# Optimization experiments

Hardware: AMD Instinct MI355X
Metric: run time of the kernel (lower is better)

Reference implementation:

```python
import jax, jax.numpy as jnp
import numpy as np

N = 100000      # nodes
E = 1600000     # edges (avg degree 16)
F_IN = 128      # node feature dim
F_E = 8         # edge feature dim
H = 4           # attention heads (layer 1)
C = 16          # hidden per head
T = 1           # target size (layer 2, heads=1, concat=False)
NEG_SLOPE = 0.2


def setup_inputs() -> dict:
    key = jax.random.key(0)
    ks = jax.random.split(key, 20)
    g = lambda k, shape, fan: (jax.random.normal(k, shape, jnp.float32) / np.sqrt(fan))
    return {
        "x": jax.random.normal(ks[0], (N, F_IN), jnp.float32),
        "edge_index": jax.random.randint(ks[1], (2, E), 0, N, dtype=jnp.int32),
        "edge_attr": jax.random.normal(ks[2], (E, F_E), jnp.float32),
        # layer 1 (in=F_IN, out=C, heads=H, concat=True, edge_dim=F_E)
        "Wl1": g(ks[3], (F_IN, H * C), F_IN),
        "bl1": jnp.zeros((H * C,), jnp.float32),
        "Wr1": g(ks[4], (F_IN, H * C), F_IN),
        "br1": jnp.zeros((H * C,), jnp.float32),
        "We1": g(ks[5], (F_E, H * C), F_E),
        "att1": g(ks[6], (H, C), C),
        "b1": jnp.zeros((H * C,), jnp.float32),
        # layer 2 (in=H*C, out=T, heads=1, concat=False, edge_dim=F_E)
        "Wl2": g(ks[7], (H * C, T), H * C),
        "bl2": jnp.zeros((T,), jnp.float32),
        "Wr2": g(ks[8], (H * C, T), H * C),
        "br2": jnp.zeros((T,), jnp.float32),
        "We2": g(ks[9], (F_E, T), F_E),
        "att2": g(ks[10], (1, T), T),
        "b2": jnp.zeros((T,), jnp.float32),
    }


def _gatv2(x, src, dst, eattr, Wl, bl, Wr, br, We, att, bias, heads, out_ch, concat, n_nodes):
    # add self loops, self-loop edge_attr = mean of edge_attr (PyG fill_value='mean')
    loop = jnp.arange(n_nodes, dtype=src.dtype)
    src_a = jnp.concatenate([src, loop])
    dst_a = jnp.concatenate([dst, loop])
    ea = jnp.concatenate(
        [eattr, jnp.broadcast_to(eattr.mean(axis=0), (n_nodes, eattr.shape[1]))], axis=0)

    xl = (x @ Wl + bl).reshape(n_nodes, heads, out_ch)   # source transform
    xr = (x @ Wr + br).reshape(n_nodes, heads, out_ch)   # target transform
    ee = (ea @ We).reshape(-1, heads, out_ch)            # edge transform (no bias)

    # GATv2: score = att . LeakyReLU(x_l[src] + x_r[dst] + W_e e)
    s = jax.nn.leaky_relu(xl[src_a] + xr[dst_a] + ee, NEG_SLOPE)  # [Ea,H,C]
    logits = jnp.einsum('ehc,hc->eh', s, att)                      # [Ea,H]

    # segment softmax over destination nodes (every node has a self loop)
    m = jax.ops.segment_max(logits, dst_a, num_segments=n_nodes)   # [N,H]
    p = jnp.exp(logits - m[dst_a])
    denom = jax.ops.segment_sum(p, dst_a, num_segments=n_nodes)
    alpha = p / denom[dst_a]                                        # [Ea,H]

    out = jax.ops.segment_sum(xl[src_a] * alpha[:, :, None], dst_a,
                              num_segments=n_nodes)                 # [N,H,C]
    out = out.reshape(n_nodes, heads * out_ch) if concat else out.mean(axis=1)
    return out + bias


def reference(x, edge_index, edge_attr, Wl1, bl1, Wr1, br1, We1, att1, b1,
              Wl2, bl2, Wr2, br2, We2, att2, b2):
    src, dst = edge_index[0], edge_index[1]
    # dropout layers are identity at eval time (training=False)
    h = _gatv2(x, src, dst, edge_attr, Wl1, bl1, Wr1, br1, We1, att1, b1,
               H, C, True, N)
    h = jax.nn.elu(h)
    out = _gatv2(h, src, dst, edge_attr, Wl2, bl2, Wr2, br2, We2, att2, b2,
                 1, T, False, N)
    return out
```

## Files before the change

kernel.cpp:

```cpp
#include <hip/hip_runtime.h>
#include <hip/hip_fp16.h>
#include <math.h>

#define N_NODES 100000
#define N_EDGES 1600000
#define N_ITEMS (N_EDGES + N_NODES)
#define F_IN 128
#define F_E 8
#define HC 64
#define NHEAD 4
#define NEG 0.2f
#define SCAN_BS 1024
#define SCAN_NB ((N_NODES + SCAN_BS - 1) / SCAN_BS)
#define MS_BLOCKS 1024
#define NEG_BIG (-3.0e38f)

union H2I { __half2 h; int i; };

__global__ void mean_sum_kernel(const float* __restrict__ ea, float* __restrict__ partials,
                                unsigned* __restrict__ deg) {
    __shared__ float sh[4][8];
    int stride = gridDim.x * blockDim.x;
    for (int i = blockIdx.x * blockDim.x + threadIdx.x; i < N_NODES; i += stride)
        deg[i] = 1u;
    float acc[8] = {0.f,0.f,0.f,0.f,0.f,0.f,0.f,0.f};
    for (int r = blockIdx.x * blockDim.x + threadIdx.x; r < N_EDGES; r += stride) {
        const float4* p = (const float4*)(ea + (size_t)r * 8);
        float4 a = p[0], b = p[1];
        acc[0] += a.x; acc[1] += a.y; acc[2] += a.z; acc[3] += a.w;
        acc[4] += b.x; acc[5] += b.y; acc[6] += b.z; acc[7] += b.w;
    }
    int wid  = threadIdx.x >> 6;
    int lane = threadIdx.x & 63;
#pragma unroll
    for (int k = 0; k < 8; k++) {
        float v = acc[k];
        for (int off = 32; off; off >>= 1) v += __shfl_down(v, off);
        if (lane == 0) sh[wid][k] = v;
    }
    __syncthreads();
    if (threadIdx.x < 8) {
        float s = sh[0][threadIdx.x] + sh[1][threadIdx.x] + sh[2][threadIdx.x] + sh[3][threadIdx.x];
        partials[blockIdx.x * 8 + threadIdx.x] = s;
    }
}

__global__ void reduce_sum8(const float* __restrict__ partials, float* __restrict__ sum8) {
    int lane = threadIdx.x;
    int c = lane & 7, g = lane >> 3;
    float s = 0.f;
    for (int b = g; b < MS_BLOCKS; b += 8) s += partials[b * 8 + c];
    s += __shfl_xor(s, 8);
    s += __shfl_xor(s, 16);
    s += __shfl_xor(s, 32);
    if (lane < 8) sum8[lane] = s;
}

__global__ void hist_kernel(const int* __restrict__ dst, unsigned* __restrict__ deg) {
    int e = blockIdx.x * blockDim.x + threadIdx.x;
    if (e < N_EDGES) atomicAdd(&deg[dst[e]], 1u);
}

__global__ void scan1(const unsigned* __restrict__ deg, unsigned* __restrict__ local_inc,
                      unsigned* __restrict__ bsum) {
    __shared__ unsigned wsum[16];
    int i = blockIdx.x * SCAN_BS + threadIdx.x;
    int lane = threadIdx.x & 63;
    int wid  = threadIdx.x >> 6;
    unsigned v = (i < N_NODES) ? deg[i] : 0u;
    unsigned sc = v;
#pragma unroll
    for (int off = 1; off < 64; off <<= 1) {
        unsigned t = __shfl_up(sc, off);
        if (lane >= off) sc += t;
    }
    if (lane == 63) wsum[wid] = sc;
    __syncthreads();
    if (threadIdx.x < 16) {
        unsigned w = wsum[threadIdx.x];
#pragma unroll
        for (int off = 1; off < 16; off <<= 1) {
            unsigned t = __shfl_up(w, off);
            if ((int)threadIdx.x >= off) w += t;
        }
        wsum[threadIdx.x] = w;
    }
    __syncthreads();
    unsigned base = wid ? wsum[wid - 1] : 0u;
    sc += base;
    if (i < N_NODES) local_inc[i] = sc;
    if (threadIdx.x == SCAN_BS - 1) bsum[blockIdx.x] = sc;
}

__global__ void scan2(unsigned* __restrict__ bsum) {
    __shared__ unsigned tmp[128];
    int t = threadIdx.x;
    unsigned v = (t < SCAN_NB) ? bsum[t] : 0u;
    tmp[t] = v;
    __syncthreads();
    for (int off = 1; off < 128; off <<= 1) {
        unsigned add = (t >= off) ? tmp[t - off] : 0u;
        __syncthreads();
        tmp[t] += add;
        __syncthreads();
    }
    if (t < SCAN_NB) bsum[t] = tmp[t] - v;
}

__global__ void scan3(const unsigned* __restrict__ local_inc, const unsigned* __restrict__ deg,
                      const unsigned* __restrict__ bsum,
                      unsigned* __restrict__ row_start, unsigned* __restrict__ next) {
    int i = blockIdx.x * blockDim.x + threadIdx.x;
    if (i >= N_NODES) return;
    unsigned v = local_inc[i] - deg[i] + bsum[i / SCAN_BS];
    row_start[i] = v;
    next[i] = v;
}

__global__ void scatter_kernel(const int* __restrict__ src, const int* __restrict__ dst,
                               const float* __restrict__ ea, const float* __restrict__ sum8,
                               const float* __restrict__ We2,
                               unsigned* __restrict__ next,
                               int* __restrict__ sorted_src, __half* __restrict__ seah,
                               float* __restrict__ see2) {
    int item = blockIdx.x * blockDim.x + threadIdx.x;
    if (item >= N_ITEMS) return;
    int s, d;
    float4 a, b;
    if (item < N_EDGES) {
        s = src[item]; d = dst[item];
        const float4* p = (const float4*)(ea + (size_t)item * 8);
        a = p[0]; b = p[1];
    } else {
        s = d = item - N_EDGES;
        const float inv = 1.0f / N_EDGES;
        a = make_float4(sum8[0]*inv, sum8[1]*inv, sum8[2]*inv, sum8[3]*inv);
        b = make_float4(sum8[4]*inv, sum8[5]*inv, sum8[6]*inv, sum8[7]*inv);
    }
    float ee2 = a.x*We2[0] + a.y*We2[1] + a.z*We2[2] + a.w*We2[3]
              + b.x*We2[4] + b.y*We2[5] + b.z*We2[6] + b.w*We2[7];
    unsigned pos = atomicAdd(&next[d], 1u);
    sorted_src[pos] = s;
    see2[pos] = ee2;
    H2I p0, p1, p2, p3;
    p0.h = __floats2half2_rn(a.x, a.y);
    p1.h = __floats2half2_rn(a.z, a.w);
    p2.h = __floats2half2_rn(b.x, b.y);
    p3.h = __floats2half2_rn(b.z, b.w);
    *(int4*)(seah + (size_t)pos * 8) = make_int4(p0.i, p1.i, p2.i, p3.i);
}

__global__ __launch_bounds__(256) void gemm1_kernel(
        const float* __restrict__ x,
        const float* __restrict__ Wl, const float* __restrict__ bl,
        const float* __restrict__ Wr, const float* __restrict__ br,
        __half* __restrict__ xlh, float* __restrict__ xr) {
    __shared__ float xs_t[F_IN][36];
    int t = threadIdx.x & 31;
    int g = threadIdx.x >> 5;
    const float* Wsel = (t < 16) ? Wl : Wr;
    const float* bsel = (t < 16) ? bl : br;
    int jc = (t < 16) ? 4 * t : 4 * t - HC;
    float4 bias = *(const float4*)(bsel + jc);

    int n0 = blockIdx.x * 32;
    int row = threadIdx.x >> 3;
    int cq  = threadIdx.x & 7;
#pragma unroll
    for (int r = 0; r < 4; r++) {
        int c = cq * 4 + r * 32;
        float4 v = *(const float4*)(x + (size_t)(n0 + row) * F_IN + c);
        xs_t[c + 0][row] = v.x;
        xs_t[c + 1][row] = v.y;
        xs_t[c + 2][row] = v.z;
        xs_t[c + 3][row] = v.w;
    }
    __syncthreads();
    int nb = g * 4;
    float4 a0 = bias, a1 = bias, a2 = bias, a3 = bias;
#pragma unroll 4
    for (int k = 0; k < F_IN; k++) {
        float4 w  = *(const float4*)(Wsel + k * HC + jc);
        float4 xv = *(const float4*)&xs_t[k][nb];
        a0.x += w.x * xv.x; a0.y += w.y * xv.x; a0.z += w.z * xv.x; a0.w += w.w * xv.x;
        a1.x += w.x * xv.y; a1.y += w.y * xv.y; a1.z += w.z * xv.y; a1.w += w.w * xv.y;
        a2.x += w.x * xv.z; a2.y += w.y * xv.z; a2.z += w.z * xv.z; a2.w += w.w * xv.z;
        a3.x += w.x * xv.w; a3.y += w.y * xv.w; a3.z += w.z * xv.w; a3.w += w.w * xv.w;
    }
    if (t < 16) {
        float4 arr[4] = {a0, a1, a2, a3};
#pragma unroll
        for (int r = 0; r < 4; r++) {
            H2I u0, u1;
            u0.h = __floats2half2_rn(arr[r].x, arr[r].y);
            u1.h = __floats2half2_rn(arr[r].z, arr[r].w);
            *(int2*)(xlh + (size_t)(n0 + nb + r) * HC + jc) = make_int2(u0.i, u1.i);
        }
    } else {
        *(float4*)(xr + (size_t)(n0 + nb + 0) * HC + jc) = a0;
        *(float4*)(xr + (size_t)(n0 + nb + 1) * HC + jc) = a1;
        *(float4*)(xr + (size_t)(n0 + nb + 2) * HC + jc) = a2;
        *(float4*)(xr + (size_t)(n0 + nb + 3) * HC + jc) = a3;
    }
}

__device__ __forceinline__ float4 sea_lo(const int4& r) {
    H2I h0, h1; h0.i = r.x; h1.i = r.y;
    float2 f0 = __half22float2(h0.h), f1 = __half22float2(h1.h);
    return make_float4(f0.x, f0.y, f1.x, f1.y);
}
__device__ __forceinline__ float4 sea_hi(const int4& r) {
    H2I h2, h3; h2.i = r.z; h3.i = r.w;
    float2 f2 = __half22float2(h2.h), f3 = __half22float2(h3.h);
    return make_float4(f2.x, f2.y, f3.x, f3.y);
}
__device__ __forceinline__ float4 xl_f(const int2& w) {
    H2I u0, u1; u0.i = w.x; u1.i = w.y;
    float2 g0 = __half22float2(u0.h), g1 = __half22float2(u1.h);
    return make_float4(g0.x, g0.y, g1.x, g1.y);
}

__device__ __forceinline__ void edge_update(const float4* __restrict__ we,
                                            const float4& attv, const float4& xrv,
                                            bool valid, const float4& ea0, const float4& ea1,
                                            const float4& xlv,
                                            float& m, float& den, float4& acc) {
    float4 v;
    v.x = xlv.x + xrv.x + ea0.x*we[0].x + ea0.y*we[1].x + ea0.z*we[2].x + ea0.w*we[3].x
                        + ea1.x*we[4].x + ea1.y*we[5].x + ea1.z*we[6].x + ea1.w*we[7].x;
    v.y = xlv.y + xrv.y + ea0.x*we[0].y + ea0.y*we[1].y + ea0.z*we[2].y + ea0.w*we[3].y
                        + ea1.x*we[4].y + ea1.y*we[5].y + ea1.z*we[6].y + ea1.w*we[7].y;
    v.z = xlv.z + xrv.z + ea0.x*we[0].z + ea0.y*we[1].z + ea0.z*we[2].z + ea0.w*we[3].z
                        + ea1.x*we[4].z + ea1.y*we[5].z + ea1.z*we[6].z + ea1.w*we[7].z;
    v.w = xlv.w + xrv.w + ea0.x*we[0].w + ea0.y*we[1].w + ea0.z*we[2].w + ea0.w*we[3].w
                        + ea1.x*we[4].w + ea1.y*we[5].w + ea1.z*we[6].w + ea1.w*we[7].w;
    v.x = fmaxf(v.x, NEG * v.x);
    v.y = fmaxf(v.y, NEG * v.y);
    v.z = fmaxf(v.z, NEG * v.z);
    v.w = fmaxf(v.w, NEG * v.w);
    float prod = v.x*attv.x + v.y*attv.y + v.z*attv.z + v.w*attv.w;
    prod += __shfl_xor(prod, 1);
    prod += __shfl_xor(prod, 2);
    float logit = valid ? prod : NEG_BIG;
    float mnew  = fmaxf(m, logit);
    float scale = __expf(m - mnew);
    float p     = valid ? __expf(logit - mnew) : 0.f;
    den   = den   * scale + p;
    acc.x = acc.x * scale + p * xlv.x;
    acc.y = acc.y * scale + p * xlv.y;
    acc.z = acc.z * scale + p * xlv.z;
    acc.w = acc.w * scale + p * xlv.w;
    m = mnew;
}

#define GAT1_BLOCKS 2048
__global__ __launch_bounds__(256) void gat1_kernel(
                            const unsigned* __restrict__ row_start, const unsigned* __restrict__ deg,
                            const int* __restrict__ ssrc, const __half* __restrict__ seah,
                            const float* __restrict__ We1, const float* __restrict__ att1,
                            const float* __restrict__ b1,
                            const __half* __restrict__ xlh, const float* __restrict__ xr,
                            const float* __restrict__ Wl2, const float* __restrict__ bl2,
                            const float* __restrict__ Wr2, const float* __restrict__ br2,
                            float* __restrict__ xl2, float* __restrict__ xr2) {
    int wave  = blockIdx.x * (blockDim.x >> 6) + (threadIdx.x >> 6);
    int nwave = GAT1_BLOCKS * 4;
    int lane = threadIdx.x & 63;
    int g  = lane >> 4;
    int cl = lane & 15;

    float4 we[8];
#pragma unroll
    for (int k = 0; k < 8; k++) we[k] = *(const float4*)(We1 + k * HC + 4 * cl);
    float4 attv = *(const float4*)(att1 + 4 * cl);
    float4 b1v  = *(const float4*)(b1 + 4 * cl);
    float4 wl2v = *(const float4*)(Wl2 + 4 * cl);
    float4 wr2v = *(const float4*)(Wr2 + 4 * cl);
    float bl2s = bl2[0], br2s = br2[0];

    for (int node = wave; node < N_NODES; node += nwave) {
        unsigned start = row_start[node];
        unsigned cnt   = deg[node];
        unsigned cm1   = cnt - 1;
        float4 xrv = *(const float4*)(xr + (size_t)node * HC + 4 * cl);

        float mA = NEG_BIG, denA = 0.f, mB = NEG_BIG, denB = 0.f;
        float4 accA = make_float4(0.f,0.f,0.f,0.f), accB = make_float4(0.f,0.f,0.f,0.f);

#define IDXA(J) (start + min((J) + (unsigned)g, cm1))
#define IDXB(J) (start + min((J) + 4u + (unsigned)g, cm1))
        int sA = ssrc[IDXA(0u)], sB = ssrc[IDXB(0u)];
        int4 spA = *(const int4*)(seah + (size_t)IDXA(0u) * 8);
        int4 spB = *(const int4*)(seah + (size_t)IDXB(0u) * 8);
        int2 xpA = *(const int2*)(xlh + (size_t)sA * HC + 4 * cl);
        int2 xpB = *(const int2*)(xlh + (size_t)sB * HC + 4 * cl);
        int sA_n = ssrc[IDXA(8u)], sB_n = ssrc[IDXB(8u)];

        for (unsigned j = 0; j < cnt; j += 8) {
            float4 e0A = sea_lo(spA), e1A = sea_hi(spA), xA = xl_f(xpA);
            float4 e0B = sea_lo(spB), e1B = sea_hi(spB), xB = xl_f(xpB);
            bool vA = (j + g) < cnt, vB = (j + 4 + g) < cnt;
            if (j + 8 < cnt) {
                spA = *(const int4*)(seah + (size_t)IDXA(j + 8) * 8);
                spB = *(const int4*)(seah + (size_t)IDXB(j + 8) * 8);
                xpA = *(const int2*)(xlh + (size_t)sA_n * HC + 4 * cl);
                xpB = *(const int2*)(xlh + (size_t)sB_n * HC + 4 * cl);
                if (j + 16 < cnt) {
                    sA_n = ssrc[IDXA(j + 16)];
                    sB_n = ssrc[IDXB(j + 16)];
                }
            }
            edge_update(we, attv, xrv, vA, e0A, e1A, xA, mA, denA, accA);
            edge_update(we, attv, xrv, vB, e0B, e1B, xB, mB, denB, accB);
        }
#undef IDXA
#undef IDXB

        float m = fmaxf(mA, mB);
        float sAc = __expf(mA - m), sBc = __expf(mB - m);
        float den = denA * sAc + denB * sBc;
        float4 acc;
        acc.x = accA.x * sAc + accB.x * sBc;
        acc.y = accA.y * sAc + accB.y * sBc;
        acc.z = accA.z * sAc + accB.z * sBc;
        acc.w = accA.w * sAc + accB.w * sBc;

        float M = m;
        M = fmaxf(M, __shfl_xor(M, 16));
        M = fmaxf(M, __shfl_xor(M, 32));
        float gs = __expf(m - M);
        den *= gs; acc.x *= gs; acc.y *= gs; acc.z *= gs; acc.w *= gs;
        den   += __shfl_xor(den, 16);   den   += __shfl_xor(den, 32);
        acc.x += __shfl_xor(acc.x, 16); acc.x += __shfl_xor(acc.x, 32);
        acc.y += __shfl_xor(acc.y, 16); acc.y += __shfl_xor(acc.y, 32);
        acc.z += __shfl_xor(acc.z, 16); acc.z += __shfl_xor(acc.z, 32);
        acc.w += __shfl_xor(acc.w, 16); acc.w += __shfl_xor(acc.w, 32);

        float inv_den = 1.f / den;
        float4 o;
        o.x = acc.x * inv_den + b1v.x;
        o.y = acc.y * inv_den + b1v.y;
        o.z = acc.z * inv_den + b1v.z;
        o.w = acc.w * inv_den + b1v.w;
        o.x = o.x > 0.f ? o.x : __expf(o.x) - 1.f;
        o.y = o.y > 0.f ? o.y : __expf(o.y) - 1.f;
        o.z = o.z > 0.f ? o.z : __expf(o.z) - 1.f;
        o.w = o.w > 0.f ? o.w : __expf(o.w) - 1.f;
        float sl = o.x*wl2v.x + o.y*wl2v.y + o.z*wl2v.z + o.w*wl2v.w;
        float sr = o.x*wr2v.x + o.y*wr2v.y + o.z*wr2v.z + o.w*wr2v.w;
#pragma unroll
        for (int off = 1; off <= 8; off <<= 1) {
            sl += __shfl_xor(sl, off);
            sr += __shfl_xor(sr, off);
        }
        if (lane == 0) {
            xl2[node] = sl + bl2s;
            xr2[node] = sr + br2s;
        }
    }
}

#define GAT2_BLOCKS 2048
__global__ __launch_bounds__(256) void gat2_kernel(
                            const unsigned* __restrict__ row_start, const unsigned* __restrict__ deg,
                            const int* __restrict__ sorted_src, const float* __restrict__ see2,
                            const float* __restrict__ att2,
                            const float* __restrict__ xl2, const float* __restrict__ xr2,
                            const float* __restrict__ b2, float* __restrict__ out) {
    int wave  = blockIdx.x * (blockDim.x >> 6) + (threadIdx.x >> 6);
    int nwave = GAT2_BLOCKS * 4;
    int lane = threadIdx.x & 63;
    float a2 = att2[0];
    float b2s = b2[0];
    for (int node = wave; node < N_NODES; node += nwave) {
        unsigned start = row_start[node];
        unsigned cnt   = deg[node];
        float xrv = xr2[node];
        float m = -INFINITY, den = 0.f, num = 0.f;
        for (unsigned base = 0; base < cnt; base += 64) {
            unsigned idx = base + lane;
            float logit = -INFINITY, xv = 0.f;
            if (idx < cnt) {
                int s = sorted_src[start + idx];
                float ee = see2[start + idx];
                xv = xl2[s];
                float v = xv + xrv + ee;
                v = fmaxf(v, NEG * v);
                logit = a2 * v;
            }
            float mm = logit;
            for (int off = 1; off < 64; off <<= 1) mm = fmaxf(mm, __shfl_xor(mm, off));
            float mnew = fmaxf(m, mm);
            float p  = (idx < cnt) ? __expf(logit - mnew) : 0.f;
            float pn = p * xv;
            for (int off = 1; off < 64; off <<= 1) {
                p  += __shfl_xor(p, off);
                pn += __shfl_xor(pn, off);
            }
            float scale = __expf(m - mnew);
            den = den * scale + p;
            num = num * scale + pn;
            m = mnew;
        }
        if (lane == 0) out[node] = num / den + b2s;
    }
}

extern "C" void kernel_launch(void* const* d_in, const int* in_sizes, int n_in,
                              void* d_out, int out_size, void* d_ws, size_t ws_size,
                              hipStream_t stream) {
    const float* x    = (const float*)d_in[0];
    const int*   ei   = (const int*)d_in[1];
    const float* ea   = (const float*)d_in[2];
    const float* Wl1  = (const float*)d_in[3];
    const float* bl1  = (const float*)d_in[4];
    const float* Wr1  = (const float*)d_in[5];
    const float* br1  = (const float*)d_in[6];
    const float* We1  = (const float*)d_in[7];
    const float* att1 = (const float*)d_in[8];
    const float* b1   = (const float*)d_in[9];
    const float* Wl2  = (const float*)d_in[10];
    const float* bl2  = (const float*)d_in[11];
    const float* Wr2  = (const float*)d_in[12];
    const float* br2  = (const float*)d_in[13];
    const float* We2  = (const float*)d_in[14];
    const float* att2 = (const float*)d_in[15];
    const float* b2   = (const float*)d_in[16];

    const int* src = ei;
    const int* dst = ei + N_EDGES;

    float* W = (float*)d_ws;
    size_t o = 0;
    float*    sum8      = W + o;               o += 8;
    float*    partials  = W + o;               o += MS_BLOCKS * 8;
    unsigned* deg       = (unsigned*)(W + o);  o += N_NODES;
    unsigned* local_inc = (unsigned*)(W + o);  o += N_NODES;
    unsigned* bsum      = (unsigned*)(W + o);  o += 128;
    unsigned* row_start = (unsigned*)(W + o);  o += N_NODES;
    unsigned* next      = (unsigned*)(W + o);  o += N_NODES;
    int*      ssrc      = (int*)(W + o);       o += N_ITEMS;
    float*    see2      = W + o;               o += N_ITEMS;
    o = (o + 3) & ~(size_t)3;
    __half*   seah      = (__half*)(W + o);    o += (size_t)N_ITEMS * 4;
    __half*   xl1h      = (__half*)(W + o);    o += (size_t)N_NODES * (HC / 2);
    float*    xr1       = W + o;               o += (size_t)N_NODES * HC;
    float*    xl2       = W + o;               o += N_NODES;
    float*    xr2       = W + o;               o += N_NODES;

    mean_sum_kernel<<<MS_BLOCKS, 256, 0, stream>>>(ea, partials, deg);
    reduce_sum8<<<1, 64, 0, stream>>>(partials, sum8);
    hist_kernel<<<(N_EDGES + 255) / 256, 256, 0, stream>>>(dst, deg);
    scan1<<<SCAN_NB, SCAN_BS, 0, stream>>>(deg, local_inc, bsum);
    scan2<<<1, 128, 0, stream>>>(bsum);
    scan3<<<(N_NODES + 255) / 256, 256, 0, stream>>>(local_inc, deg, bsum, row_start, next);
    scatter_kernel<<<(N_ITEMS + 255) / 256, 256, 0, stream>>>(
        src, dst, ea, sum8, We2, next, ssrc, seah, see2);
    gemm1_kernel<<<N_NODES / 32, 256, 0, stream>>>(x, Wl1, bl1, Wr1, br1, xl1h, xr1);
    gat1_kernel<<<GAT1_BLOCKS, 256, 0, stream>>>(
        row_start, deg, ssrc, seah, We1, att1, b1, xl1h, xr1,
        Wl2, bl2, Wr2, br2, xl2, xr2);
    gat2_kernel<<<GAT2_BLOCKS, 256, 0, stream>>>(
        row_start, deg, ssrc, see2, att2, xl2, xr2, b2, (float*)d_out);
}
```

Before: 452.3 us.

## Fuse preprocessing kernels, drop online softmax max, pack edge records, remap GAT waves

Folds the degree histogram into the edge-attr mean kernel, the partials reduction into scan1, and scan2/scan3 into one kernel, with a memset replacing explicit degree initialisation. That cuts the number of launches. Source index and layer-2 edge term are packed into one 8-byte record, so each edge needs one load instead of two. Both GAT kernels now compute softmax without the running max, trading numerical safety for fewer exp and rescale operations. Layer 1 maps one node per wave over the full grid, and layer 2 handles four nodes per wave with 16 lanes each, using nontemporal loads for edge streams.

```diff
diff --git a/kernel.cpp b/kernel.cpp
--- a/kernel.cpp
+++ b/kernel.cpp
@@ -6,29 +6,43 @@
 #define N_EDGES 1600000
 #define N_ITEMS (N_EDGES + N_NODES)
 #define F_IN 128
-#define F_E 8
 #define HC 64
-#define NHEAD 4
 #define NEG 0.2f
 #define SCAN_BS 1024
 #define SCAN_NB ((N_NODES + SCAN_BS - 1) / SCAN_BS)
 #define MS_BLOCKS 1024
-#define NEG_BIG (-3.0e38f)
 
 union H2I { __half2 h; int i; };
-
-__global__ void mean_sum_kernel(const float* __restrict__ ea, float* __restrict__ partials,
-                                unsigned* __restrict__ deg) {
+typedef int v2i __attribute__((ext_vector_type(2)));
+typedef int v4i __attribute__((ext_vector_type(4)));
+
+__device__ __forceinline__ float4 h4_to_f4(v2i w) {
+    H2I u0, u1; u0.i = w.x; u1.i = w.y;
+    float2 a = __half22float2(u0.h), b = __half22float2(u1.h);
+    return make_float4(a.x, a.y, b.x, b.y);
+}
+__device__ __forceinline__ float4 h8_lo(v4i r) {
+    H2I h0, h1; h0.i = r.x; h1.i = r.y;
+    float2 f0 = __half22float2(h0.h), f1 = __half22float2(h1.h);
+    return make_float4(f0.x, f0.y, f1.x, f1.y);
+}
+__device__ __forceinline__ float4 h8_hi(v4i r) {
+    H2I h2, h3; h2.i = r.z; h3.i = r.w;
+    float2 f2 = __half22float2(h2.h), f3 = __half22float2(h3.h);
+    return make_float4(f2.x, f2.y, f3.x, f3.y);
+}
+
+__global__ void mean_sum_kernel(const float* __restrict__ ea, const int* __restrict__ dst,
+                                float* __restrict__ partials, unsigned* __restrict__ deg) {
     __shared__ float sh[4][8];
     int stride = gridDim.x * blockDim.x;
-    for (int i = blockIdx.x * blockDim.x + threadIdx.x; i < N_NODES; i += stride)
-        deg[i] = 1u;
     float acc[8] = {0.f,0.f,0.f,0.f,0.f,0.f,0.f,0.f};
     for (int r = blockIdx.x * blockDim.x + threadIdx.x; r < N_EDGES; r += stride) {
         const float4* p = (const float4*)(ea + (size_t)r * 8);
         float4 a = p[0], b = p[1];
         acc[0] += a.x; acc[1] += a.y; acc[2] += a.z; acc[3] += a.w;
         acc[4] += b.x; acc[5] += b.y; acc[6] += b.z; acc[7] += b.w;
+        atomicAdd(&deg[dst[r]], 1u);
     }
     int wid  = threadIdx.x >> 6;
     int lane = threadIdx.x & 63;
@@ -45,29 +59,24 @@
     }
 }
 
-__global__ void reduce_sum8(const float* __restrict__ partials, float* __restrict__ sum8) {
-    int lane = threadIdx.x;
-    int c = lane & 7, g = lane >> 3;
-    float s = 0.f;
-    for (int b = g; b < MS_BLOCKS; b += 8) s += partials[b * 8 + c];
-    s += __shfl_xor(s, 8);
-    s += __shfl_xor(s, 16);
-    s += __shfl_xor(s, 32);
-    if (lane < 8) sum8[lane] = s;
-}
-
-__global__ void hist_kernel(const int* __restrict__ dst, unsigned* __restrict__ deg) {
-    int e = blockIdx.x * blockDim.x + threadIdx.x;
-    if (e < N_EDGES) atomicAdd(&deg[dst[e]], 1u);
-}
-
 __global__ void scan1(const unsigned* __restrict__ deg, unsigned* __restrict__ local_inc,
-                      unsigned* __restrict__ bsum) {
+                      unsigned* __restrict__ bsum,
+                      const float* __restrict__ partials, float* __restrict__ sum8) {
+    if (blockIdx.x == 0 && threadIdx.x < 64) {
+        int lane = threadIdx.x;
+        int c = lane & 7, g = lane >> 3;
+        float s = 0.f;
+        for (int b = g; b < MS_BLOCKS; b += 8) s += partials[b * 8 + c];
+        s += __shfl_xor(s, 8);
+        s += __shfl_xor(s, 16);
+        s += __shfl_xor(s, 32);
+        if (lane < 8) sum8[lane] = s;
+    }
     __shared__ unsigned wsum[16];
     int i = blockIdx.x * SCAN_BS + threadIdx.x;
     int lane = threadIdx.x & 63;
     int wid  = threadIdx.x >> 6;
-    unsigned v = (i < N_NODES) ? deg[i] : 0u;
+    unsigned v = (i < N_NODES) ? (deg[i] + 1u) : 0u;
     unsigned sc = v;
 #pragma unroll
     for (int off = 1; off < 64; off <<= 1) {
@@ -92,27 +101,25 @@
     if (threadIdx.x == SCAN_BS - 1) bsum[blockIdx.x] = sc;
 }
 
-__global__ void scan2(unsigned* __restrict__ bsum) {
+__global__ void scan23(const unsigned* __restrict__ local_inc, const unsigned* __restrict__ deg,
+                       const unsigned* __restrict__ bsum,
+                       unsigned* __restrict__ row_start, unsigned* __restrict__ next) {
     __shared__ unsigned tmp[128];
     int t = threadIdx.x;
-    unsigned v = (t < SCAN_NB) ? bsum[t] : 0u;
-    tmp[t] = v;
+    if (t < 128) tmp[t] = (t < SCAN_NB) ? bsum[t] : 0u;
     __syncthreads();
     for (int off = 1; off < 128; off <<= 1) {
-        unsigned add = (t >= off) ? tmp[t - off] : 0u;
+        unsigned add = 0u;
+        if (t < 128 && t >= off) add = tmp[t - off];
         __syncthreads();
-        tmp[t] += add;
+        if (t < 128) tmp[t] += add;
         __syncthreads();
     }
-    if (t < SCAN_NB) bsum[t] = tmp[t] - v;
-}
-
-__global__ void scan3(const unsigned* __restrict__ local_inc, const unsigned* __restrict__ deg,
-                      const unsigned* __restrict__ bsum,
-                      unsigned* __restrict__ row_start, unsigned* __restrict__ next) {
-    int i = blockIdx.x * blockDim.x + threadIdx.x;
+    int i = blockIdx.x * blockDim.x + t;
     if (i >= N_NODES) return;
-    unsigned v = local_inc[i] - deg[i] + bsum[i / SCAN_BS];
+    int b = i >> 10;
+    unsigned base = b ? tmp[b - 1] : 0u;
+    unsigned v = local_inc[i] - (deg[i] + 1u) + base;
     row_start[i] = v;
     next[i] = v;
 }
@@ -121,8 +128,7 @@
                                const float* __restrict__ ea, const float* __restrict__ sum8,
                                const float* __restrict__ We2,
                                unsigned* __restrict__ next,
-                               int* __restrict__ sorted_src, __half* __restrict__ seah,
-                               float* __restrict__ see2) {
+                               int* __restrict__ rec, __half* __restrict__ seah) {
     int item = blockIdx.x * blockDim.x + threadIdx.x;
     if (item >= N_ITEMS) return;
     int s, d;
@@ -140,8 +146,8 @@
     float ee2 = a.x*We2[0] + a.y*We2[1] + a.z*We2[2] + a.w*We2[3]
               + b.x*We2[4] + b.y*We2[5] + b.z*We2[6] + b.w*We2[7];
     unsigned pos = atomicAdd(&next[d], 1u);
-    sorted_src[pos] = s;
-    see2[pos] = ee2;
+    v2i rr; rr.x = s; rr.y = __float_as_int(ee2);
+    *(v2i*)(rec + (size_t)pos * 2) = rr;
     H2I p0, p1, p2, p3;
     p0.h = __floats2half2_rn(a.x, a.y);
     p1.h = __floats2half2_rn(a.z, a.w);
@@ -204,27 +210,11 @@
     }
 }
 
-__device__ __forceinline__ float4 sea_lo(const int4& r) {
-    H2I h0, h1; h0.i = r.x; h1.i = r.y;
-    float2 f0 = __half22float2(h0.h), f1 = __half22float2(h1.h);
-    return make_float4(f0.x, f0.y, f1.x, f1.y);
-}
-__device__ __forceinline__ float4 sea_hi(const int4& r) {
-    H2I h2, h3; h2.i = r.z; h3.i = r.w;
-    float2 f2 = __half22float2(h2.h), f3 = __half22float2(h3.h);
-    return make_float4(f2.x, f2.y, f3.x, f3.y);
-}
-__device__ __forceinline__ float4 xl_f(const int2& w) {
-    H2I u0, u1; u0.i = w.x; u1.i = w.y;
-    float2 g0 = __half22float2(u0.h), g1 = __half22float2(u1.h);
-    return make_float4(g0.x, g0.y, g1.x, g1.y);
-}
-
-__device__ __forceinline__ void edge_update(const float4* __restrict__ we,
-                                            const float4& attv, const float4& xrv,
-                                            bool valid, const float4& ea0, const float4& ea1,
-                                            const float4& xlv,
-                                            float& m, float& den, float4& acc) {
+__device__ __forceinline__ void edge_update_nm(const float4* __restrict__ we,
+                                               const float4& attv, const float4& xrv,
+                                               bool valid, const float4& ea0, const float4& ea1,
+                                               const float4& xlv,
+                                               float& den, float4& acc) {
     float4 v;
     v.x = xlv.x + xrv.x + ea0.x*we[0].x + ea0.y*we[1].x + ea0.z*we[2].x + ea0.w*we[3].x
                         + ea1.x*we[4].x + ea1.y*we[5].x + ea1.z*we[6].x + ea1.w*we[7].x;
@@ -241,169 +231,139 @@
     float prod = v.x*attv.x + v.y*attv.y + v.z*attv.z + v.w*attv.w;
     prod += __shfl_xor(prod, 1);
     prod += __shfl_xor(prod, 2);
-    float logit = valid ? prod : NEG_BIG;
-    float mnew  = fmaxf(m, logit);
-    float scale = __expf(m - mnew);
-    float p     = valid ? __expf(logit - mnew) : 0.f;
-    den   = den   * scale + p;
-    acc.x = acc.x * scale + p * xlv.x;
-    acc.y = acc.y * scale + p * xlv.y;
-    acc.z = acc.z * scale + p * xlv.z;
-    acc.w = acc.w * scale + p * xlv.w;
-    m = mnew;
-}
-
-#define GAT1_BLOCKS 2048
-__global__ __launch_bounds__(256) void gat1_kernel(
-                            const unsigned* __restrict__ row_start, const unsigned* __restrict__ deg,
-                            const int* __restrict__ ssrc, const __half* __restrict__ seah,
+    float p = valid ? __expf(prod) : 0.f;
+    den   += p;
+    acc.x += p * xlv.x;
+    acc.y += p * xlv.y;
+    acc.z += p * xlv.z;
+    acc.w += p * xlv.w;
+}
+
+__global__ void gat1_kernel(const unsigned* __restrict__ row_start, const unsigned* __restrict__ deg,
+                            const int* __restrict__ rec, const __half* __restrict__ seah,
                             const float* __restrict__ We1, const float* __restrict__ att1,
                             const float* __restrict__ b1,
                             const __half* __restrict__ xlh, const float* __restrict__ xr,
                             const float* __restrict__ Wl2, const float* __restrict__ bl2,
                             const float* __restrict__ Wr2, const float* __restrict__ br2,
                             float* __restrict__ xl2, float* __restrict__ xr2) {
-    int wave  = blockIdx.x * (blockDim.x >> 6) + (threadIdx.x >> 6);
-    int nwave = GAT1_BLOCKS * 4;
+    int node = blockIdx.x * (blockDim.x >> 6) + (threadIdx.x >> 6);
     int lane = threadIdx.x & 63;
+    if (node >= N_NODES) return;
     int g  = lane >> 4;
     int cl = lane & 15;
+    unsigned start = row_start[node];
+    unsigned cnt   = deg[node] + 1u;
+    unsigned cm1   = cnt - 1u;
 
     float4 we[8];
 #pragma unroll
     for (int k = 0; k < 8; k++) we[k] = *(const float4*)(We1 + k * HC + 4 * cl);
     float4 attv = *(const float4*)(att1 + 4 * cl);
+    float4 xrv  = *(const float4*)(xr + (size_t)node * HC + 4 * cl);
+
+    float denA = 0.f, denB = 0.f;
+    float4 accA = make_float4(0.f,0.f,0.f,0.f), accB = make_float4(0.f,0.f,0.f,0.f);
+
+#define IDXA(J) (start + min((J) + (unsigned)g, cm1))
+#define IDXB(J) (start + min((J) + 4u + (unsigned)g, cm1))
+    unsigned iA = IDXA(0u), iB = IDXB(0u);
+    v2i rA = __builtin_nontemporal_load((const v2i*)(rec + (size_t)iA * 2));
+    v2i rB = __builtin_nontemporal_load((const v2i*)(rec + (size_t)iB * 2));
+    v4i spA = __builtin_nontemporal_load((const v4i*)(seah + (size_t)iA * 8));
+    v4i spB = __builtin_nontemporal_load((const v4i*)(seah + (size_t)iB * 8));
+    v2i xpA = *(const v2i*)(xlh + (size_t)rA.x * HC + 4 * cl);
+    v2i xpB = *(const v2i*)(xlh + (size_t)rB.x * HC + 4 * cl);
+
+    for (unsigned j = 0; j < cnt; j += 8) {
+        float4 e0A = h8_lo(spA), e1A = h8_hi(spA), xA = h4_to_f4(xpA);
+        float4 e0B = h8_lo(spB), e1B = h8_hi(spB), xB = h4_to_f4(xpB);
+        bool vA = (j + g) < cnt, vB = (j + 4 + g) < cnt;
+        if (j + 8 < cnt) {
+            iA = IDXA(j + 8); iB = IDXB(j + 8);
+            rA = __builtin_nontemporal_load((const v2i*)(rec + (size_t)iA * 2));
+            rB = __builtin_nontemporal_load((const v2i*)(rec + (size_t)iB * 2));
+            spA = __builtin_nontemporal_load((const v4i*)(seah + (size_t)iA * 8));
+            spB = __builtin_nontemporal_load((const v4i*)(seah + (size_t)iB * 8));
+            xpA = *(const v2i*)(xlh + (size_t)rA.x * HC + 4 * cl);
+            xpB = *(const v2i*)(xlh + (size_t)rB.x * HC + 4 * cl);
+        }
+        edge_update_nm(we, attv, xrv, vA, e0A, e1A, xA, denA, accA);
+        edge_update_nm(we, attv, xrv, vB, e0B, e1B, xB, denB, accB);
+    }
+#undef IDXA
+#undef IDXB
+
+    float den = denA + denB;
+    float4 acc;
+    acc.x = accA.x + accB.x;
+    acc.y = accA.y + accB.y;
+    acc.z = accA.z + accB.z;
+    acc.w = accA.w + accB.w;
+
+    den   += __shfl_xor(den, 16);   den   += __shfl_xor(den, 32);
+    acc.x += __shfl_xor(acc.x, 16); acc.x += __shfl_xor(acc.x, 32);
+    acc.y += __shfl_xor(acc.y, 16); acc.y += __shfl_xor(acc.y, 32);
+    acc.z += __shfl_xor(acc.z, 16); acc.z += __shfl_xor(acc.z, 32);
+    acc.w += __shfl_xor(acc.w, 16); acc.w += __shfl_xor(acc.w, 32);
+
     float4 b1v  = *(const float4*)(b1 + 4 * cl);
     float4 wl2v = *(const float4*)(Wl2 + 4 * cl);
     float4 wr2v = *(const float4*)(Wr2 + 4 * cl);
-    float bl2s = bl2[0], br2s = br2[0];
-
-    for (int node = wave; node < N_NODES; node += nwave) {
-        unsigned start = row_start[node];
-        unsigned cnt   = deg[node];
-        unsigned cm1   = cnt - 1;
-        float4 xrv = *(const float4*)(xr + (size_t)node * HC + 4 * cl);
-
-        float mA = NEG_BIG, denA = 0.f, mB = NEG_BIG, denB = 0.f;
-        float4 accA = make_float4(0.f,0.f,0.f,0.f), accB = make_float4(0.f,0.f,0.f,0.f);
-
-#define IDXA(J) (start + min((J) + (unsigned)g, cm1))
-#define IDXB(J) (start + min((J) + 4u + (unsigned)g, cm1))
-        int sA = ssrc[IDXA(0u)], sB = ssrc[IDXB(0u)];
-        int4 spA = *(const int4*)(seah + (size_t)IDXA(0u) * 8);
-        int4 spB = *(const int4*)(seah + (size_t)IDXB(0u) * 8);
-        int2 xpA = *(const int2*)(xlh + (size_t)sA * HC + 4 * cl);
-        int2 xpB = *(const int2*)(xlh + (size_t)sB * HC + 4 * cl);
-        int sA_n = ssrc[IDXA(8u)], sB_n = ssrc[IDXB(8u)];
-
-        for (unsigned j = 0; j < cnt; j += 8) {
-            float4 e0A = sea_lo(spA), e1A = sea_hi(spA), xA = xl_f(xpA);
-            float4 e0B = sea_lo(spB), e1B = sea_hi(spB), xB = xl_f(xpB);
-            bool vA = (j + g) < cnt, vB = (j + 4 + g) < cnt;
-            if (j + 8 < cnt) {
-                spA = *(const int4*)(seah + (size_t)IDXA(j + 8) * 8);
-                spB = *(const int4*)(seah + (size_t)IDXB(j + 8) * 8);
-                xpA = *(const int2*)(xlh + (size_t)sA_n * HC + 4 * cl);
-                xpB = *(const int2*)(xlh + (size_t)sB_n * HC + 4 * cl);
-                if (j + 16 < cnt) {
-                    sA_n = ssrc[IDXA(j + 16)];
-                    sB_n = ssrc[IDXB(j + 16)];
-                }
-            }
-            edge_update(we, attv, xrv, vA, e0A, e1A, xA, mA, denA, accA);
-            edge_update(we, attv, xrv, vB, e0B, e1B, xB, mB, denB, accB);
-        }
-#undef IDXA
-#undef IDXB
-
-        float m = fmaxf(mA, mB);
-        float sAc = __expf(mA - m), sBc = __expf(mB - m);
-        float den = denA * sAc + denB * sBc;
-        float4 acc;
-        acc.x = accA.x * sAc + accB.x * sBc;
-        acc.y = accA.y * sAc + accB.y * sBc;
-        acc.z = accA.z * sAc + accB.z * sBc;
-        acc.w = accA.w * sAc + accB.w * sBc;
-
-        float M = m;
-        M = fmaxf(M, __shfl_xor(M, 16));
-        M = fmaxf(M, __shfl_xor(M, 32));
-        float gs = __expf(m - M);
-        den *= gs; acc.x *= gs; acc.y *= gs; acc.z *= gs; acc.w *= gs;
-        den   += __shfl_xor(den, 16);   den   += __shfl_xor(den, 32);
-        acc.x += __shfl_xor(acc.x, 16); acc.x += __shfl_xor(acc.x, 32);
-        acc.y += __shfl_xor(acc.y, 16); acc.y += __shfl_xor(acc.y, 32);
-        acc.z += __shfl_xor(acc.z, 16); acc.z += __shfl_xor(acc.z, 32);
-        acc.w += __shfl_xor(acc.w, 16); acc.w += __shfl_xor(acc.w, 32);
-
-        float inv_den = 1.f / den;
-        float4 o;
-        o.x = acc.x * inv_den + b1v.x;
-        o.y = acc.y * inv_den + b1v.y;
-        o.z = acc.z * inv_den + b1v.z;
-        o.w = acc.w * inv_den + b1v.w;
-        o.x = o.x > 0.f ? o.x : __expf(o.x) - 1.f;
-        o.y = o.y > 0.f ? o.y : __expf(o.y) - 1.f;
-        o.z = o.z > 0.f ? o.z : __expf(o.z) - 1.f;
-        o.w = o.w > 0.f ? o.w : __expf(o.w) - 1.f;
-        float sl = o.x*wl2v.x + o.y*wl2v.y + o.z*wl2v.z + o.w*wl2v.w;
-        float sr = o.x*wr2v.x + o.y*wr2v.y + o.z*wr2v.z + o.w*wr2v.w;
-#pragma unroll
-        for (int off = 1; off <= 8; off <<= 1) {
-            sl += __shfl_xor(sl, off);
-            sr += __shfl_xor(sr, off);
-        }
-        if (lane == 0) {
-            xl2[node] = sl + bl2s;
-            xr2[node] = sr + br2s;
-        }
-    }
-}
-
-#define GAT2_BLOCKS 2048
+    float inv_den = 1.f / den;
+    float4 o;
+    o.x = acc.x * inv_den + b1v.x;
+    o.y = acc.y * inv_den + b1v.y;
+    o.z = acc.z * inv_den + b1v.z;
+    o.w = acc.w * inv_den + b1v.w;
+    o.x = o.x > 0.f ? o.x : __expf(o.x) - 1.f;
+    o.y = o.y > 0.f ? o.y : __expf(o.y) - 1.f;
+    o.z = o.z > 0.f ? o.z : __expf(o.z) - 1.f;
+    o.w = o.w > 0.f ? o.w : __expf(o.w) - 1.f;
+    float sl = o.x*wl2v.x + o.y*wl2v.y + o.z*wl2v.z + o.w*wl2v.w;
+    float sr = o.x*wr2v.x + o.y*wr2v.y + o.z*wr2v.z + o.w*wr2v.w;
+#pragma unroll
+    for (int off = 1; off <= 8; off <<= 1) {
+        sl += __shfl_xor(sl, off);
+        sr += __shfl_xor(sr, off);
+    }
+    if (lane == 0) {
+        xl2[node] = sl + bl2[0];
+        xr2[node] = sr + br2[0];
+    }
+}
+
 __global__ __launch_bounds__(256) void gat2_kernel(
-                            const unsigned* __restrict__ row_start, const unsigned* __restrict__ deg,
-                            const int* __restrict__ sorted_src, const float* __restrict__ see2,
-                            const float* __restrict__ att2,
-                            const float* __restrict__ xl2, const float* __restrict__ xr2,
-                            const float* __restrict__ b2, float* __restrict__ out) {
-    int wave  = blockIdx.x * (blockDim.x >> 6) + (threadIdx.x >> 6);
-    int nwave = GAT2_BLOCKS * 4;
+        const unsigned* __restrict__ row_start, const unsigned* __restrict__ deg,
+        const int* __restrict__ rec, const float* __restrict__ att2,
+        const float* __restrict__ xl2, const float* __restrict__ xr2,
+        const float* __restrict__ b2, float* __restrict__ out) {
+    int wave = threadIdx.x >> 6;
     int lane = threadIdx.x & 63;
-    float a2 = att2[0];
-    float b2s = b2[0];
-    for (int node = wave; node < N_NODES; node += nwave) {
-        unsigned start = row_start[node];
-        unsigned cnt   = deg[node];
-        float xrv = xr2[node];
-        float m = -INFINITY, den = 0.f, num = 0.f;
-        for (unsigned base = 0; base < cnt; base += 64) {
-            unsigned idx = base + lane;
-            float logit = -INFINITY, xv = 0.f;
-            if (idx < cnt) {
-                int s = sorted_src[start + idx];
-                float ee = see2[start + idx];
-                xv = xl2[s];
-                float v = xv + xrv + ee;
-                v = fmaxf(v, NEG * v);
-                logit = a2 * v;
-            }
-            float mm = logit;
-            for (int off = 1; off < 64; off <<= 1) mm = fmaxf(mm, __shfl_xor(mm, off));
-            float mnew = fmaxf(m, mm);
-            float p  = (idx < cnt) ? __expf(logit - mnew) : 0.f;
-            float pn = p * xv;
-            for (int off = 1; off < 64; off <<= 1) {
-                p  += __shfl_xor(p, off);
-                pn += __shfl_xor(pn, off);
-            }
-            float scale = __expf(m - mnew);
-            den = den * scale + p;
-            num = num * scale + pn;
-            m = mnew;
-        }
-        if (lane == 0) out[node] = num / den + b2s;
-    }
+    int sub  = lane >> 4;
+    int l    = lane & 15;
+    int node = (blockIdx.x * 4 + wave) * 4 + sub;
+    unsigned start = row_start[node];
+    unsigned cnt   = deg[node] + 1u;
+    float xrv = xr2[node];
+    float a2  = att2[0];
+    float den = 0.f, num = 0.f;
+    for (unsigned idx = (unsigned)l; idx < cnt; idx += 16) {
+        v2i r = __builtin_nontemporal_load((const v2i*)(rec + (size_t)(start + idx) * 2));
+        float ee = __int_as_float(r.y);
+        float xv = xl2[r.x];
+        float v = xv + xrv + ee;
+        v = fmaxf(v, NEG * v);
+        float p = __expf(a2 * v);
+        den += p;
+        num += p * xv;
+    }
+#pragma unroll
+    for (int off = 1; off <= 8; off <<= 1) {
+        den += __shfl_xor(den, off);
+        num += __shfl_xor(num, off);
+    }
+    if (l == 0) out[node] = num / den + b2[0];
 }
 
 extern "C" void kernel_launch(void* const* d_in, const int* in_sizes, int n_in,
@@ -439,27 +399,24 @@
     unsigned* bsum      = (unsigned*)(W + o);  o += 128;
     unsigned* row_start = (unsigned*)(W + o);  o += N_NODES;
     unsigned* next      = (unsigned*)(W + o);  o += N_NODES;
-    int*      ssrc      = (int*)(W + o);       o += N_ITEMS;
-    float*    see2      = W + o;               o += N_ITEMS;
     o = (o + 3) & ~(size_t)3;
+    int*      rec       = (int*)(W + o);       o += (size_t)N_ITEMS * 2;
     __half*   seah      = (__half*)(W + o);    o += (size_t)N_ITEMS * 4;
-    __half*   xl1h      = (__half*)(W + o);    o += (size_t)N_NODES * (HC / 2);
+    __half*   xlh       = (__half*)(W + o);    o += (size_t)N_NODES * (HC/2);
     float*    xr1       = W + o;               o += (size_t)N_NODES * HC;
     float*    xl2       = W + o;               o += N_NODES;
     float*    xr2       = W + o;               o += N_NODES;
 
-    mean_sum_kernel<<<MS_BLOCKS, 256, 0, stream>>>(ea, partials, deg);
-    reduce_sum8<<<1, 64, 0, stream>>>(partials, sum8);
-    hist_kernel<<<(N_EDGES + 255) / 256, 256, 0, stream>>>(dst, deg);
-    scan1<<<SCAN_NB, SCAN_BS, 0, stream>>>(deg, local_inc, bsum);
-    scan2<<<1, 128, 0, stream>>>(bsum);
-    scan3<<<(N_NODES + 255) / 256, 256, 0, stream>>>(local_inc, deg, bsum, row_start, next);
+    hipMemsetAsync(deg, 0, (size_t)N_NODES * sizeof(unsigned), stream);
+    mean_sum_kernel<<<MS_BLOCKS, 256, 0, stream>>>(ea, dst, partials, deg);
+    scan1<<<SCAN_NB, SCAN_BS, 0, stream>>>(deg, local_inc, bsum, partials, sum8);
+    scan23<<<(N_NODES + 255) / 256, 256, 0, stream>>>(local_inc, deg, bsum, row_start, next);
     scatter_kernel<<<(N_ITEMS + 255) / 256, 256, 0, stream>>>(
-        src, dst, ea, sum8, We2, next, ssrc, seah, see2);
-    gemm1_kernel<<<N_NODES / 32, 256, 0, stream>>>(x, Wl1, bl1, Wr1, br1, xl1h, xr1);
-    gat1_kernel<<<GAT1_BLOCKS, 256, 0, stream>>>(
-        row_start, deg, ssrc, seah, We1, att1, b1, xl1h, xr1,
+        src, dst, ea, sum8, We2, next, rec, seah);
+    gemm1_kernel<<<N_NODES / 32, 256, 0, stream>>>(x, Wl1, bl1, Wr1, br1, xlh, xr1);
+    gat1_kernel<<<(N_NODES + 3) / 4, 256, 0, stream>>>(
+        row_start, deg, rec, seah, We1, att1, b1, xlh, xr1,
         Wl2, bl2, Wr2, br2, xl2, xr2);
-    gat2_kernel<<<GAT2_BLOCKS, 256, 0, stream>>>(
-        row_start, deg, ssrc, see2, att2, xl2, xr2, b2, (float*)d_out);
-}
+    gat2_kernel<<<N_NODES / 16, 256, 0, stream>>>(
+        row_start, deg, rec, att2, xl2, xr2, b2, (float*)d_out);
+}
```

Result: no change. 445.2 us (-1.6%).
